# Kernel optimization log

Measured on AMD Instinct MI355X. Metric: run time of the kernel, lower is better.

The kernel has to match this reference:

```python
import jax, jax.numpy as jnp
import numpy as np

LN_EPS = 1e-5

def _layernorm(z, g, b):
    m = jnp.mean(z, axis=-1, keepdims=True)
    v = jnp.mean(jnp.square(z - m), axis=-1, keepdims=True)
    return (z - m) / jnp.sqrt(v + LN_EPS) * g + b

def setup_inputs() -> dict:
    key = jax.random.key(0)
    ks = jax.random.split(key, 8)
    B, N, C, H = 16, 1024, 384, 6
    Dff = 4 * C
    s = 0.02
    return {
        "x": jax.random.normal(ks[0], (B, N, C), dtype=jnp.float32),
        "ln1_g": jnp.ones((C,), jnp.float32),
        "ln1_b": jnp.zeros((C,), jnp.float32),
        "qkv_w": jax.random.normal(ks[1], (3 * C, C), jnp.float32) * s,
        "proj_w": jax.random.normal(ks[2], (C, C), jnp.float32) * s,
        "proj_b": jnp.zeros((C,), jnp.float32),
        "gate_h": jnp.ones((H,), jnp.float32),
        "ln2_g": jnp.ones((C,), jnp.float32),
        "ln2_b": jnp.zeros((C,), jnp.float32),
        "fc1_w": jax.random.normal(ks[3], (Dff, C), jnp.float32) * s,
        "fc1_b": jnp.zeros((Dff,), jnp.float32),
        "fc2_w": jax.random.normal(ks[4], (C, Dff), jnp.float32) * s,
        "fc2_b": jnp.zeros((C,), jnp.float32),
        "gate_mlp": jnp.ones((Dff,), jnp.float32),
    }

def reference(x, ln1_g, ln1_b, qkv_w, proj_w, proj_b, gate_h,
              ln2_g, ln2_b, fc1_w, fc1_b, fc2_w, fc2_b, gate_mlp):
    B, N, C = x.shape
    H = gate_h.shape[0]
    Dh = C // H
    scale = Dh ** -0.5

    # Attention branch
    h = _layernorm(x, ln1_g, ln1_b)
    qkv = (h @ qkv_w.T).reshape(B, N, 3, H, Dh).transpose(2, 0, 3, 1, 4)  # [3,B,H,N,Dh]
    q, k, v = qkv[0], qkv[1], qkv[2]
    attn = jax.nn.softmax(jnp.einsum('bhnd,bhmd->bhnm', q, k) * scale, axis=-1)  # [B,H,N,N]
    o = jnp.einsum('bhnm,bhmd->bhnd', attn, v)            # [B,H,N,Dh]
    o = o.transpose(0, 2, 1, 3) * gate_h[None, None, :, None]  # per-head gate
    o = o.reshape(B, N, C) @ proj_w.T + proj_b
    x = x + o

    # MLP branch (exact GELU, per-neuron gate)
    h2 = _layernorm(x, ln2_g, ln2_b)
    m = jax.nn.gelu(h2 @ fc1_w.T + fc1_b, approximate=False) * gate_mlp
    x = x + (m @ fc2_w.T + fc2_b)
    return x
```

## Files before the change

### kernel.cpp

```cpp
#include <hip/hip_runtime.h>
#include <hip/hip_bf16.h>
#include <cstdint>
#include <cstddef>

#define B_   16
#define N_   1024
#define C_   384
#define H_   6
#define DFF_ 1536
#define R_   16384

typedef __attribute__((ext_vector_type(8))) __bf16 bf16x8;
typedef __attribute__((ext_vector_type(4))) float  f32x4;
typedef __attribute__((ext_vector_type(8))) unsigned short u16x8;
typedef __attribute__((ext_vector_type(4))) unsigned short u16x4;

__device__ __forceinline__ float bf2f(unsigned short u){
    unsigned int x = ((unsigned int)u) << 16;
    return __builtin_bit_cast(float, x);
}
__device__ __forceinline__ unsigned short f2bf(float f){
    return __builtin_bit_cast(unsigned short, __float2bfloat16(f));
}
__device__ __forceinline__ unsigned int cvt_pk_bf16(float a, float b){
    unsigned int r;
    asm("v_cvt_pk_bf16_f32 %0, %1, %2" : "=v"(r) : "v"(a), "v"(b));
    return r;
}
__device__ __forceinline__ float fast_exp2(float x){
    float r;
    asm("v_exp_f32 %0, %1" : "=v"(r) : "v"(x));
    return r;
}
__device__ __forceinline__ void gload16(const void* g, void* l){
    __builtin_amdgcn_global_load_lds(
        (const __attribute__((address_space(1))) unsigned int*)g,
        (__attribute__((address_space(3))) unsigned int*)l, 16, 0, 0);
}
__device__ __forceinline__ float gelu_f(float u){
    float z  = fabsf(u) * 0.70710678118654752f;
    float t  = __builtin_amdgcn_rcpf(1.0f + 0.47047f*z);
    float e  = __expf(-z*z);
    float p  = t*(0.3480242f + t*(-0.0958798f + t*0.7478556f));
    float er = 1.0f - p*e;
    return 0.5f*u*(1.0f + copysignf(er, u));
}
__device__ __forceinline__ float ldv(const float* p, size_t i){ return p[i]; }
__device__ __forceinline__ float ldv(const __hip_bfloat16* p, size_t i){ return __bfloat162float(p[i]); }

__global__ __launch_bounds__(256) void ln1_cvt_kernel(
    const float* __restrict__ x, const float* __restrict__ g,
    const float* __restrict__ b, __hip_bfloat16* __restrict__ out,
    const float* __restrict__ i0, __hip_bfloat16* __restrict__ o0, int n0,
    const float* __restrict__ i1, __hip_bfloat16* __restrict__ o1, int n1,
    const float* __restrict__ i2, __hip_bfloat16* __restrict__ o2, int n2,
    const float* __restrict__ i3, __hip_bfloat16* __restrict__ o3, int n3)
{
    if (blockIdx.x < 4096){
        const int lane = threadIdx.x & 63;
        const int wave = threadIdx.x >> 6;
        const int row  = blockIdx.x*4 + wave;
        const float* xr = x + (size_t)row*C_;
        float v[6];
        float s = 0.f;
        #pragma unroll
        for (int i=0;i<6;i++){ v[i] = xr[lane + i*64]; s += v[i]; }
        #pragma unroll
        for (int m=1;m<64;m<<=1) s += __shfl_xor(s, m);
        const float mean = s * (1.0f/C_);
        float sq = 0.f;
        #pragma unroll
        for (int i=0;i<6;i++){ float d = v[i]-mean; sq += d*d; }
        #pragma unroll
        for (int m=1;m<64;m<<=1) sq += __shfl_xor(sq, m);
        const float rstd = rsqrtf(sq*(1.0f/C_) + 1e-5f);
        #pragma unroll
        for (int i=0;i<6;i++){
            int c = lane + i*64;
            out[(size_t)row*C_ + c] = __float2bfloat16((v[i]-mean)*rstd*g[c] + b[c]);
        }
    } else {
        const int total = n0+n1+n2+n3;
        for (int i = (blockIdx.x-4096)*blockDim.x + threadIdx.x; i < total; i += 1024*blockDim.x){
            int k = i;
            if (k < n0){ o0[k] = __float2bfloat16(i0[k]); continue; }
            k -= n0;
            if (k < n1){ o1[k] = __float2bfloat16(i1[k]); continue; }
            k -= n1;
            if (k < n2){ o2[k] = __float2bfloat16(i2[k]); continue; }
            k -= n2;
            o3[k] = __float2bfloat16(i3[k]);
        }
    }
}

template<typename T>
__global__ __launch_bounds__(256) void ln_kernel(
    const T* __restrict__ x, const float* __restrict__ g,
    const float* __restrict__ b, __hip_bfloat16* __restrict__ out)
{
    const int lane = threadIdx.x & 63;
    const int wave = threadIdx.x >> 6;
    const int row  = blockIdx.x*4 + wave;
    const T* xr = x + (size_t)row*C_;
    float v[6];
    float s = 0.f;
    #pragma unroll
    for (int i=0;i<6;i++){ v[i] = ldv(xr, lane + i*64); s += v[i]; }
    #pragma unroll
    for (int m=1;m<64;m<<=1) s += __shfl_xor(s, m);
    const float mean = s * (1.0f/C_);
    float sq = 0.f;
    #pragma unroll
    for (int i=0;i<6;i++){ float d = v[i]-mean; sq += d*d; }
    #pragma unroll
    for (int m=1;m<64;m<<=1) sq += __shfl_xor(sq, m);
    const float rstd = rsqrtf(sq*(1.0f/C_) + 1e-5f);
    #pragma unroll
    for (int i=0;i<6;i++){
        int c = lane + i*64;
        out[(size_t)row*C_ + c] = __float2bfloat16((v[i]-mean)*rstd*g[c] + b[c]);
    }
}

enum { EPI_QKV=0, EPI_PROJ=1, EPI_FC2=3 };


template<int EPI, int NCOLS>
__global__ __launch_bounds__(256, 2) void gemm_wres(
    const __hip_bfloat16* __restrict__ A,
    const __hip_bfloat16* __restrict__ Wt,
    const float* __restrict__ bias,
    const float* __restrict__ resid,
    const float* __restrict__ gate,
    __hip_bfloat16* __restrict__ outb)
{
    constexpr int NB = NCOLS/64;
    constexpr int G  = 24;
    __shared__ __align__(16) unsigned short As[4][128*32];
    __shared__ __align__(16) unsigned short Bs[64*384];
    const int t = threadIdx.x;
    const int l = t & 63;
    const int w = t >> 6;
    const int X  = blockIdx.x & 7;
    const int j8 = blockIdx.x >> 3;
    const int rb = X*8 + j8 / NB;
    const int cb = j8 % NB;

    #pragma unroll
    for (int j=0;j<12;j++){
        const int L     = (w*12 + j)*1024 + l*16;
        const int row   = L / 768;
        const int cbyte = L - row*768;
        const int scol  = (cbyte ^ ((row&7)<<4)) >> 1;
        gload16(Wt + (size_t)(cb*64 + row)*384 + scol, (char*)&Bs[0] + L);
    }
    const int sgcol = (((l&3) - ((l>>3)&3)) & 3) * 8;
    const size_t arow0 = (size_t)rb*256 + w*32 + (l>>2);
    auto STAGEA = [&](int g){
        const int rt = g/12, s = g - rt*12;
        #pragma unroll
        for (int c=0;c<2;c++)
            gload16(A + (arow0 + rt*128 + c*16)*384 + s*32 + sgcol,
                    (char*)&As[g&3][0] + w*2048 + c*1024 + l*16);
    };
    STAGEA(0); STAGEA(1); STAGEA(2);
    asm volatile("s_waitcnt vmcnt(6)" ::: "memory");
    __builtin_amdgcn_s_barrier();

    #pragma unroll
    for (int rt=0; rt<2; ++rt){
        f32x4 acc[2][4];
        #pragma unroll
        for (int i=0;i<2;i++)
            #pragma unroll
            for (int jj=0;jj<4;jj++) acc[i][jj] = (f32x4){0.f,0.f,0.f,0.f};

        #pragma unroll
        for (int s=0; s<12; ++s){
            const int g = rt*12 + s;
            if (g <= G-3)      asm volatile("s_waitcnt vmcnt(4)" ::: "memory");
            else if (g == G-2) asm volatile("s_waitcnt vmcnt(2)" ::: "memory");
            else               asm volatile("s_waitcnt vmcnt(0)" ::: "memory");
            const char* as = (const char*)&As[g&3][0] + w*2048;
            bf16x8 af[2], bw[4];
            #pragma unroll
            for (int i=0;i<2;i++){
                const int r  = i*16 + (l&15);
                const int sl = ((l>>4) + ((r>>1)&3)) & 3;
                af[i] = *(const bf16x8*)(as + r*64 + sl*16);
            }
            #pragma unroll
            for (int i=0;i<4;i++){
                const int r = i*16 + (l&15);
                bw[i] = *(const bf16x8*)((const char*)&Bs[0] + r*768
                             + ((s*64 + (l>>4)*16) ^ ((r&7)<<4)));
            }
            #pragma unroll
            for (int mi=0;mi<2;mi++)
                #pragma unroll
                for (int ni=0;ni<4;ni++)
                    acc[mi][ni] = __builtin_amdgcn_mfma_f32_16x16x32_bf16(af[mi], bw[ni], acc[mi][ni], 0,0,0);
            asm volatile("s_waitcnt lgkmcnt(0)" ::: "memory");
            if (g+3 < G) STAGEA(g+3);
        }
        const int rowBase = rb*256 + rt*128 + w*32;
        if constexpr (EPI==EPI_QKV){
            unsigned short* ob = (unsigned short*)outb;
            #pragma unroll
            for (int ni=0; ni<4; ni++){
                const int col = cb*64 + ni*16 + (l&15);
                const int p = col/384, rem = col - p*384;
                const int hh = rem>>6, d = rem&63;
                #pragma unroll
                for (int mi=0; mi<2; mi++){
                    const int row0 = rowBase + mi*16 + (l>>4)*4;
                    const int bb = row0>>10, n = row0&1023;
                    if (p==2){
                        u16x4 pk;
                        #pragma unroll
                        for (int jj=0;jj<4;jj++) pk[jj] = f2bf(acc[mi][ni][jj]);
                        *(u16x4*)(ob + (size_t)2*6291456 + ((size_t)(bb*H_+hh)*64 + d)*1024 + n) = pk;
                    } else {
                        #pragma unroll
                        for (int jj=0;jj<4;jj++)
                            ob[(((size_t)((p*16+bb)*6+hh))<<16) + ((size_t)(n+jj)<<6) + d] = f2bf(acc[mi][ni][jj]);
                    }
                }
            }
        } else {
            #pragma unroll
            for (int ni=0; ni<4; ni++){
                const int col = cb*64 + ni*16 + (l&15);
                #pragma unroll
                for (int mi=0; mi<2; mi++){
                    #pragma unroll
                    for (int jj=0;jj<4;jj++){
                        const int row = rowBase + mi*16 + (l>>4)*4 + jj;
                        const size_t idx = (size_t)row*NCOLS + col;
                        outb[idx] = __float2bfloat16(resid[idx] + acc[mi][ni][jj] + bias[col]);
                    }
                }
            }
        }
    }
}

template<int NCOLS>
__global__ __launch_bounds__(256, 2) void gemm_wres4(
    const __hip_bfloat16* __restrict__ A,
    const __hip_bfloat16* __restrict__ Wt,
    const float* __restrict__ bias,
    const float* __restrict__ gate,
    __hip_bfloat16* __restrict__ outb)
{
    constexpr int NB = NCOLS/64;
    __shared__ __align__(16) unsigned short As[4][128*32];
    __shared__ __align__(16) unsigned short Bs[64*384];
    const int t = threadIdx.x;
    const int l = t & 63;
    const int w = t >> 6;
    const int X  = blockIdx.x & 7;
    const int j8 = blockIdx.x >> 3;
    const int rb = X*16 + j8 / NB;
    const int cb = j8 % NB;

    #pragma unroll
    for (int j=0;j<12;j++){
        const int L     = (w*12 + j)*1024 + l*16;
        const int row   = L / 768;
        const int cbyte = L - row*768;
        const int scol  = (cbyte ^ ((row&7)<<4)) >> 1;
        gload16(Wt + (size_t)(cb*64 + row)*384 + scol, (char*)&Bs[0] + L);
    }
    const int sgcol = (((l&3) - ((l>>3)&3)) & 3) * 8;
    const size_t arow0 = (size_t)rb*128 + w*32 + (l>>2);
    auto STAGEA = [&](int g){
        #pragma unroll
        for (int c=0;c<2;c++)
            gload16(A + (arow0 + c*16)*384 + g*32 + sgcol,
                    (char*)&As[g&3][0] + w*2048 + c*1024 + l*16);
    };
    STAGEA(0); STAGEA(1); STAGEA(2);
    asm volatile("s_waitcnt vmcnt(6)" ::: "memory");
    __builtin_amdgcn_s_barrier();

    f32x4 acc[2][4];
    #pragma unroll
    for (int i=0;i<2;i++)
        #pragma unroll
        for (int jj=0;jj<4;jj++) acc[i][jj] = (f32x4){0.f,0.f,0.f,0.f};

    #pragma unroll
    for (int s=0; s<12; ++s){
        if (s < 10)      asm volatile("s_waitcnt vmcnt(4)" ::: "memory");
        else if (s == 10) asm volatile("s_waitcnt vmcnt(2)" ::: "memory");
        else              asm volatile("s_waitcnt vmcnt(0)" ::: "memory");
        const char* as = (const char*)&As[s&3][0] + w*2048;
        bf16x8 af[2], bw[4];
        #pragma unroll
        for (int i=0;i<2;i++){
            const int r  = i*16 + (l&15);
            const int sl = ((l>>4) + ((r>>1)&3)) & 3;
            af[i] = *(const bf16x8*)(as + r*64 + sl*16);
        }
        #pragma unroll
        for (int i=0;i<4;i++){
            const int r = i*16 + (l&15);
            bw[i] = *(const bf16x8*)((const char*)&Bs[0] + r*768
                         + ((s*64 + (l>>4)*16) ^ ((r&7)<<4)));
        }
        #pragma unroll
        for (int mi=0;mi<2;mi++)
            #pragma unroll
            for (int ni=0;ni<4;ni++)
                acc[mi][ni] = __builtin_amdgcn_mfma_f32_16x16x32_bf16(af[mi], bw[ni], acc[mi][ni], 0,0,0);
        asm volatile("s_waitcnt lgkmcnt(0)" ::: "memory");
        if (s+3 < 12) STAGEA(s+3);
    }

    const int rowBase = rb*128 + w*32;
    #pragma unroll
    for (int ni=0; ni<4; ni++){
        const int col = cb*64 + ni*16 + (l&15);
        #pragma unroll
        for (int mi=0; mi<2; mi++){
            #pragma unroll
            for (int jj=0;jj<4;jj++){
                const int row = rowBase + mi*16 + (l>>4)*4 + jj;
                const size_t idx = (size_t)row*NCOLS + col;
                outb[idx] = __float2bfloat16(gelu_f(acc[mi][ni][jj] + bias[col]) * gate[col]);
            }
        }
    }
}

__global__ __launch_bounds__(256, 2) void gemm_wres_fc2(
    const __hip_bfloat16* __restrict__ A,
    const __hip_bfloat16* __restrict__ Wt,
    const float* __restrict__ bias,
    const __hip_bfloat16* __restrict__ residb,
    float* __restrict__ outf)
{
    constexpr int NB = 6;
    __shared__ __align__(16) unsigned short As[4][128*32];
    __shared__ __align__(16) unsigned short Bs[64*384];
    const int t = threadIdx.x;
    const int l = t & 63;
    const int w = t >> 6;
    const int X  = blockIdx.x & 7;
    const int j8 = blockIdx.x >> 3;
    const int rb = X*16 + j8 / NB;
    const int cb = j8 % NB;

    auto STAGEB = [&](int q){
        #pragma unroll
        for (int j=0;j<12;j++){
            const int L     = (w*12 + j)*1024 + l*16;
            const int row   = L / 768;
            const int cbyte = L - row*768;
            const int scol  = (cbyte ^ ((row&7)<<4)) >> 1;
            gload16(Wt + (size_t)(cb*64 + row)*1536 + q*384 + scol, (char*)&Bs[0] + L);
        }
    };
    const int sgcol = (((l&3) - ((l>>3)&3)) & 3) * 8;
    const size_t arow0 = (size_t)rb*128 + w*32 + (l>>2);
    auto STAGEA = [&](int g){
        #pragma unroll
        for (int c=0;c<2;c++)
            gload16(A + (arow0 + c*16)*1536 + g*32 + sgcol,
                    (char*)&As[g&3][0] + w*2048 + c*1024 + l*16);
    };

    STAGEB(0);
    STAGEA(0); STAGEA(1); STAGEA(2);
    asm volatile("s_waitcnt vmcnt(0)" ::: "memory");
    __builtin_amdgcn_s_barrier();
    asm volatile("" ::: "memory");

    f32x4 acc[2][4];
    #pragma unroll
    for (int i=0;i<2;i++)
        #pragma unroll
        for (int jj=0;jj<4;jj++) acc[i][jj] = (f32x4){0.f,0.f,0.f,0.f};

    for (int q=0; q<4; ++q){
        if (q > 0){
            asm volatile("s_waitcnt vmcnt(0)" ::: "memory");
            __builtin_amdgcn_s_barrier();
            asm volatile("" ::: "memory");
        }
        #pragma unroll
        for (int s=0; s<12; ++s){
            const int g = q*12 + s;
            if (s >= 3){
                if (g < 46)      asm volatile("s_waitcnt vmcnt(4)" ::: "memory");
                else if (g == 46) asm volatile("s_waitcnt vmcnt(2)" ::: "memory");
                else              asm volatile("s_waitcnt vmcnt(0)" ::: "memory");
            }
            const char* as = (const char*)&As[g&3][0] + w*2048;
            bf16x8 af[2], bw[4];
            #pragma unroll
            for (int i=0;i<2;i++){
                const int r  = i*16 + (l&15);
                const int sl = ((l>>4) + ((r>>1)&3)) & 3;
                af[i] = *(const bf16x8*)(as + r*64 + sl*16);
            }
            #pragma unroll
            for (int i=0;i<4;i++){
                const int r = i*16 + (l&15);
                bw[i] = *(const bf16x8*)((const char*)&Bs[0] + r*768
                             + ((s*64 + (l>>4)*16) ^ ((r&7)<<4)));
            }
            #pragma unroll
            for (int mi=0;mi<2;mi++)
                #pragma unroll
                for (int ni=0;ni<4;ni++)
                    acc[mi][ni] = __builtin_amdgcn_mfma_f32_16x16x32_bf16(af[mi], bw[ni], acc[mi][ni], 0,0,0);
            asm volatile("s_waitcnt lgkmcnt(0)" ::: "memory");
            if (g+3 < 48) STAGEA(g+3);
        }
        if (q < 3){
            __builtin_amdgcn_s_barrier();
            asm volatile("" ::: "memory");
            STAGEB(q+1);
        }
    }

    const int rowBase = rb*128 + w*32;
    const unsigned short* xb = (const unsigned short*)residb;
    #pragma unroll
    for (int ni=0; ni<4; ni++){
        const int col = cb*64 + ni*16 + (l&15);
        #pragma unroll
        for (int mi=0; mi<2; mi++){
            #pragma unroll
            for (int jj=0;jj<4;jj++){
                const int row = rowBase + mi*16 + (l>>4)*4 + jj;
                const size_t idx = (size_t)row*384 + col;
                outf[idx] = bf2f(xb[idx]) + acc[mi][ni][jj] + bias[col];
            }
        }
    }
}

__global__ __launch_bounds__(256) void attn_mfma(
    const __hip_bfloat16* __restrict__ qg,
    const __hip_bfloat16* __restrict__ kg,
    const __hip_bfloat16* __restrict__ vtg,
    const float* __restrict__ gate_h,
    __hip_bfloat16* __restrict__ og)
{
    __shared__ __align__(16) unsigned short Ks [3][64*64];
    __shared__ __align__(16) unsigned short Vts[3][64*64];
    const int t = threadIdx.x;
    const int l = t & 63;
    const int w = t >> 6;
    const int X  = blockIdx.x & 7;
    const int j8 = blockIdx.x >> 3;
    const int bh = X*12 + (j8 >> 3);
    const int n0 = (j8 & 7) * 128;
    const int h  = bh % H_;
    const int b  = bh / H_;
    const unsigned short* qp  = (const unsigned short*)qg  + ((size_t)bh*N_ + n0 + w*32)*64;
    const unsigned short* kp  = (const unsigned short*)kg  + (size_t)bh*N_*64;
    const unsigned short* vtp = (const unsigned short*)vtg + (size_t)bh*64*N_;

    bf16x8 qf[2][2];
    #pragma unroll
    for (int mt=0;mt<2;mt++)
        #pragma unroll
        for (int dc=0;dc<2;dc++){
            u16x8 raw = *(const u16x8*)(qp + ((size_t)(mt*16 + (l&15)))*64 + dc*32 + (l>>4)*8);
            u16x8 sc;
            #pragma unroll
            for (int j=0;j<8;j++) sc[j] = f2bf(bf2f(raw[j]) * 0.1803368801111244f);
            qf[mt][dc] = __builtin_bit_cast(bf16x8, sc);
        }

    int qk_off[4][2], pv_off[2][4];
    #pragma unroll
    for (int t4=0;t4<4;t4++){
        const int i    = l & 15;
        const int row  = 8*(i>>2) + (i&3) + 4*(t4&1) + 32*(t4>>1);
        const int swzr = (row&3) | (((row>>3)&1)<<2);
        #pragma unroll
        for (int dc=0;dc<2;dc++)
            qk_off[t4][dc] = row*128 + ((dc*64 + (l>>4)*16) ^ (swzr<<4));
    }
    #pragma unroll
    for (int nt=0;nt<4;nt++){
        const int row  = nt*16 + (l&15);
        const int swzr = (row&3) | (((row>>3)&1)<<2);
        #pragma unroll
        for (int kc=0;kc<2;kc++)
            pv_off[kc][nt] = row*128 + ((kc*64 + (l>>4)*16) ^ (swzr<<4));
    }

    const int sr  = t >> 3;
    const int sce = (t & 7) * 8;

    auto STAGE = [&](int buf, int kt){
        #pragma unroll
        for (int c=0;c<2;c++){
            const int r    = sr + c*32;
            const int swzr = (r&3) | (((r>>3)&1)<<2);
            const int col  = sce ^ (swzr<<3);
            gload16(kp  + ((size_t)(kt*64 + r))*64 + col, (char*)&Ks [buf][0] + (c*256 + t)*16);
            gload16(vtp + (size_t)r*N_ + kt*64 + col,     (char*)&Vts[buf][0] + (c*256 + t)*16);
        }
    };

    f32x4 o_acc[2][4];
    #pragma unroll
    for (int i=0;i<2;i++)
        #pragma unroll
        for (int jj=0;jj<4;jj++) o_acc[i][jj] = (f32x4){0.f,0.f,0.f,0.f};
    float rs_part[2] = {0.f, 0.f};

    STAGE(0, 0);
    STAGE(1, 1);
    int cur = 0, stb = 2;
    for (int kt=0; kt<16; kt++){
        if (kt < 15) asm volatile("s_waitcnt vmcnt(4)" ::: "memory");
        else         asm volatile("s_waitcnt vmcnt(0)" ::: "memory");
        __builtin_amdgcn_s_barrier();
        asm volatile("" ::: "memory");
        if (kt < 14){
            STAGE(stb, kt+2);
            stb = (stb+1==3) ? 0 : stb+1;
        }
        const char* ks = (const char*)&Ks[cur][0];
        const char* vs = (const char*)&Vts[cur][0];

        f32x4 s_acc[4][2];
        #pragma unroll
        for (int i=0;i<4;i++)
            #pragma unroll
            for (int jj=0;jj<2;jj++) s_acc[i][jj] = (f32x4){0.f,0.f,0.f,0.f};
        #pragma unroll
        for (int t4=0;t4<4;t4++)
            #pragma unroll
            for (int dc=0;dc<2;dc++){
                bf16x8 kf = *(const bf16x8*)(ks + qk_off[t4][dc]);
                #pragma unroll
                for (int mt=0;mt<2;mt++)
                    s_acc[t4][mt] = __builtin_amdgcn_mfma_f32_16x16x32_bf16(kf, qf[mt][dc], s_acc[t4][mt], 0,0,0);
            }
        #pragma unroll
        for (int mt=0;mt<2;mt++){
            float acc_s = 0.f;
            #pragma unroll
            for (int t4=0;t4<4;t4++){
                #pragma unroll
                for (int jj=0;jj<4;jj++){
                    float e = fast_exp2(s_acc[t4][mt][jj]);
                    s_acc[t4][mt][jj] = e;
                    acc_s += e;
                }
            }
            rs_part[mt] += acc_s;
        }
        #pragma unroll
        for (int kc=0;kc<2;kc++){
            union { unsigned int u[4]; bf16x8 v; } pu[2];
            #pragma unroll
            for (int mt=0;mt<2;mt++){
                pu[mt].u[0] = cvt_pk_bf16(s_acc[2*kc  ][mt][0], s_acc[2*kc  ][mt][1]);
                pu[mt].u[1] = cvt_pk_bf16(s_acc[2*kc  ][mt][2], s_acc[2*kc  ][mt][3]);
                pu[mt].u[2] = cvt_pk_bf16(s_acc[2*kc+1][mt][0], s_acc[2*kc+1][mt][1]);
                pu[mt].u[3] = cvt_pk_bf16(s_acc[2*kc+1][mt][2], s_acc[2*kc+1][mt][3]);
            }
            #pragma unroll
            for (int nt=0;nt<4;nt++){
                bf16x8 vf = *(const bf16x8*)(vs + pv_off[kc][nt]);
                #pragma unroll
                for (int mt=0;mt<2;mt++)
                    o_acc[mt][nt] = __builtin_amdgcn_mfma_f32_16x16x32_bf16(pu[mt].v, vf, o_acc[mt][nt], 0,0,0);
            }
        }
        cur = (cur+1==3) ? 0 : cur+1;
    }
    float rowsum[2];
    #pragma unroll
    for (int mt=0;mt<2;mt++){
        float rs = rs_part[mt];
        rs += __shfl_xor(rs, 16);
        rs += __shfl_xor(rs, 32);
        rowsum[mt] = rs;
    }
    const float gh = gate_h[h];
    float inv[2][4];
    #pragma unroll
    for (int mt=0;mt<2;mt++)
        #pragma unroll
        for (int r=0;r<4;r++)
            inv[mt][r] = gh / __shfl(rowsum[mt], (l>>4)*4 + r, 16);
    unsigned short* op = (unsigned short*)og + ((size_t)b*N_ + n0 + w*32)*C_ + h*64;
    #pragma unroll
    for (int mt=0;mt<2;mt++){
        #pragma unroll
        for (int r=0;r<4;r++){
            const int n = mt*16 + (l>>4)*4 + r;
            #pragma unroll
            for (int nt=0;nt<4;nt++)
                op[(size_t)n*C_ + nt*16 + (l&15)] = f2bf(o_acc[mt][nt][r]*inv[mt][r]);
        }
    }
}

extern "C" void kernel_launch(void* const* d_in, const int* in_sizes, int n_in,
                              void* d_out, int out_size, void* d_ws, size_t ws_size,
                              hipStream_t stream)
{
    const float* x     = (const float*)d_in[0];
    const float* ln1g  = (const float*)d_in[1];
    const float* ln1b  = (const float*)d_in[2];
    const float* qkvw  = (const float*)d_in[3];
    const float* projw = (const float*)d_in[4];
    const float* projb = (const float*)d_in[5];
    const float* gateh = (const float*)d_in[6];
    const float* ln2g  = (const float*)d_in[7];
    const float* ln2b  = (const float*)d_in[8];
    const float* fc1w  = (const float*)d_in[9];
    const float* fc1b  = (const float*)d_in[10];
    const float* fc2w  = (const float*)d_in[11];
    const float* fc2b  = (const float*)d_in[12];
    const float* gatem = (const float*)d_in[13];
    float* out = (float*)d_out;

    char* ws = (char*)d_ws;
    __hip_bfloat16* h_buf = (__hip_bfloat16*)(ws + 0);
    __hip_bfloat16* qkv   = (__hip_bfloat16*)(ws + 12582912);
    __hip_bfloat16* q_buf = qkv;
    __hip_bfloat16* k_buf = qkv + 6291456;
    __hip_bfloat16* vt_buf= qkv + 2*6291456;
    __hip_bfloat16* o_buf = (__hip_bfloat16*)(ws + 50331648);
    __hip_bfloat16* m_buf = (__hip_bfloat16*)(ws + 12582912);
    __hip_bfloat16* x1b   = (__hip_bfloat16*)(ws + 62914560);
    __hip_bfloat16* wqkv  = (__hip_bfloat16*)(ws + 88080384);
    __hip_bfloat16* wproj = (__hip_bfloat16*)(ws + 88965120);
    __hip_bfloat16* wfc1  = (__hip_bfloat16*)(ws + 89260032);
    __hip_bfloat16* wfc2  = (__hip_bfloat16*)(ws + 90439680);

    ln1_cvt_kernel<<<5120, 256, 0, stream>>>(x, ln1g, ln1b, h_buf,
                                             qkvw, wqkv, 1152*384,
                                             projw, wproj, 384*384,
                                             fc1w, wfc1, 1536*384,
                                             fc2w, wfc2, 384*1536);

    gemm_wres<EPI_QKV,1152><<<1152, 256, 0, stream>>>(h_buf, wqkv, nullptr, nullptr, nullptr, qkv);
    attn_mfma<<<768, 256, 0, stream>>>(q_buf, k_buf, vt_buf, gateh, o_buf);
    gemm_wres<EPI_PROJ,384><<<384, 256, 0, stream>>>(o_buf, wproj, projb, x, nullptr, x1b);
    ln_kernel<__hip_bfloat16><<<4096, 256, 0, stream>>>(x1b, ln2g, ln2b, h_buf);
    gemm_wres4<1536><<<3072, 256, 0, stream>>>(h_buf, wfc1, fc1b, gatem, m_buf);
    gemm_wres_fc2<<<768, 256, 0, stream>>>(m_buf, wfc2, fc2b, x1b, out);
}
```

Baseline: 169.3 us.

## Unify FC1/FC2 GEMMs into a seven-buffer A pipeline with half-width B chunks

FC1 and FC2 now share one templated GEMM kernel. The weight tile is staged in 192-wide K chunks instead of 384, which frees LDS for seven A-tile buffers and lets A be prefetched six steps ahead instead of three. The fine-grained per-step vmcnt waits are replaced by one full wait plus barriers at each B-chunk boundary. FC1 therefore gains an extra mid-loop barrier and B reload. The coarser synchronisation may stall more often even though more loads are in flight.

New measurement: 174.6 us. 3.1% more time.

```diff
diff --git a/kernel.cpp b/kernel.cpp
--- a/kernel.cpp
+++ b/kernel.cpp
@@ -123,8 +123,7 @@
     }
 }
 
-enum { EPI_QKV=0, EPI_PROJ=1, EPI_FC2=3 };
-
+enum { EPI_QKV=0, EPI_PROJ=1, EPI_FC1=2, EPI_FC2=3 };
 
 template<int EPI, int NCOLS>
 __global__ __launch_bounds__(256, 2) void gemm_wres(
@@ -246,17 +245,21 @@
     }
 }
 
-template<int NCOLS>
-__global__ __launch_bounds__(256, 2) void gemm_wres4(
+template<int EPI, int KK, int NCOLS>
+__global__ __launch_bounds__(256, 2) void gemm_wres7(
     const __hip_bfloat16* __restrict__ A,
     const __hip_bfloat16* __restrict__ Wt,
     const float* __restrict__ bias,
+    const __hip_bfloat16* __restrict__ residb,
     const float* __restrict__ gate,
-    __hip_bfloat16* __restrict__ outb)
+    __hip_bfloat16* __restrict__ outb,
+    float* __restrict__ outf)
 {
-    constexpr int NB = NCOLS/64;
-    __shared__ __align__(16) unsigned short As[4][128*32];
-    __shared__ __align__(16) unsigned short Bs[64*384];
+    constexpr int NB     = NCOLS/64;
+    constexpr int NSTEPS = KK/32;
+    constexpr int QC     = KK/192;
+    __shared__ __align__(16) unsigned short As[7][128*32];
+    __shared__ __align__(16) unsigned short Bs[64*192];
     const int t = threadIdx.x;
     const int l = t & 63;
     const int w = t >> 6;
@@ -265,115 +268,27 @@
     const int rb = X*16 + j8 / NB;
     const int cb = j8 % NB;
 
-    #pragma unroll
-    for (int j=0;j<12;j++){
-        const int L     = (w*12 + j)*1024 + l*16;
-        const int row   = L / 768;
-        const int cbyte = L - row*768;
-        const int scol  = (cbyte ^ ((row&7)<<4)) >> 1;
-        gload16(Wt + (size_t)(cb*64 + row)*384 + scol, (char*)&Bs[0] + L);
-    }
-    const int sgcol = (((l&3) - ((l>>3)&3)) & 3) * 8;
-    const size_t arow0 = (size_t)rb*128 + w*32 + (l>>2);
-    auto STAGEA = [&](int g){
-        #pragma unroll
-        for (int c=0;c<2;c++)
-            gload16(A + (arow0 + c*16)*384 + g*32 + sgcol,
-                    (char*)&As[g&3][0] + w*2048 + c*1024 + l*16);
-    };
-    STAGEA(0); STAGEA(1); STAGEA(2);
-    asm volatile("s_waitcnt vmcnt(6)" ::: "memory");
-    __builtin_amdgcn_s_barrier();
-
-    f32x4 acc[2][4];
-    #pragma unroll
-    for (int i=0;i<2;i++)
-        #pragma unroll
-        for (int jj=0;jj<4;jj++) acc[i][jj] = (f32x4){0.f,0.f,0.f,0.f};
-
-    #pragma unroll
-    for (int s=0; s<12; ++s){
-        if (s < 10)      asm volatile("s_waitcnt vmcnt(4)" ::: "memory");
-        else if (s == 10) asm volatile("s_waitcnt vmcnt(2)" ::: "memory");
-        else              asm volatile("s_waitcnt vmcnt(0)" ::: "memory");
-        const char* as = (const char*)&As[s&3][0] + w*2048;
-        bf16x8 af[2], bw[4];
-        #pragma unroll
-        for (int i=0;i<2;i++){
-            const int r  = i*16 + (l&15);
-            const int sl = ((l>>4) + ((r>>1)&3)) & 3;
-            af[i] = *(const bf16x8*)(as + r*64 + sl*16);
-        }
-        #pragma unroll
-        for (int i=0;i<4;i++){
-            const int r = i*16 + (l&15);
-            bw[i] = *(const bf16x8*)((const char*)&Bs[0] + r*768
-                         + ((s*64 + (l>>4)*16) ^ ((r&7)<<4)));
-        }
-        #pragma unroll
-        for (int mi=0;mi<2;mi++)
-            #pragma unroll
-            for (int ni=0;ni<4;ni++)
-                acc[mi][ni] = __builtin_amdgcn_mfma_f32_16x16x32_bf16(af[mi], bw[ni], acc[mi][ni], 0,0,0);
-        asm volatile("s_waitcnt lgkmcnt(0)" ::: "memory");
-        if (s+3 < 12) STAGEA(s+3);
-    }
-
-    const int rowBase = rb*128 + w*32;
-    #pragma unroll
-    for (int ni=0; ni<4; ni++){
-        const int col = cb*64 + ni*16 + (l&15);
-        #pragma unroll
-        for (int mi=0; mi<2; mi++){
-            #pragma unroll
-            for (int jj=0;jj<4;jj++){
-                const int row = rowBase + mi*16 + (l>>4)*4 + jj;
-                const size_t idx = (size_t)row*NCOLS + col;
-                outb[idx] = __float2bfloat16(gelu_f(acc[mi][ni][jj] + bias[col]) * gate[col]);
-            }
-        }
-    }
-}
-
-__global__ __launch_bounds__(256, 2) void gemm_wres_fc2(
-    const __hip_bfloat16* __restrict__ A,
-    const __hip_bfloat16* __restrict__ Wt,
-    const float* __restrict__ bias,
-    const __hip_bfloat16* __restrict__ residb,
-    float* __restrict__ outf)
-{
-    constexpr int NB = 6;
-    __shared__ __align__(16) unsigned short As[4][128*32];
-    __shared__ __align__(16) unsigned short Bs[64*384];
-    const int t = threadIdx.x;
-    const int l = t & 63;
-    const int w = t >> 6;
-    const int X  = blockIdx.x & 7;
-    const int j8 = blockIdx.x >> 3;
-    const int rb = X*16 + j8 / NB;
-    const int cb = j8 % NB;
-
     auto STAGEB = [&](int q){
         #pragma unroll
-        for (int j=0;j<12;j++){
-            const int L     = (w*12 + j)*1024 + l*16;
-            const int row   = L / 768;
-            const int cbyte = L - row*768;
+        for (int j=0;j<6;j++){
+            const int L     = (w*6 + j)*1024 + l*16;
+            const int row   = L / 384;
+            const int cbyte = L - row*384;
             const int scol  = (cbyte ^ ((row&7)<<4)) >> 1;
-            gload16(Wt + (size_t)(cb*64 + row)*1536 + q*384 + scol, (char*)&Bs[0] + L);
+            gload16(Wt + (size_t)(cb*64 + row)*KK + q*192 + scol, (char*)&Bs[0] + L);
         }
     };
     const int sgcol = (((l&3) - ((l>>3)&3)) & 3) * 8;
     const size_t arow0 = (size_t)rb*128 + w*32 + (l>>2);
-    auto STAGEA = [&](int g){
+    auto STAGEA = [&](int g, int buf){
         #pragma unroll
         for (int c=0;c<2;c++)
-            gload16(A + (arow0 + c*16)*1536 + g*32 + sgcol,
-                    (char*)&As[g&3][0] + w*2048 + c*1024 + l*16);
+            gload16(A + (arow0 + c*16)*KK + g*32 + sgcol,
+                    (char*)&As[buf][0] + w*2048 + c*1024 + l*16);
     };
 
     STAGEB(0);
-    STAGEA(0); STAGEA(1); STAGEA(2);
+    STAGEA(0,0); STAGEA(1,1); STAGEA(2,2); STAGEA(3,3); STAGEA(4,4); STAGEA(5,5);
     asm volatile("s_waitcnt vmcnt(0)" ::: "memory");
     __builtin_amdgcn_s_barrier();
     asm volatile("" ::: "memory");
@@ -384,61 +299,75 @@
         #pragma unroll
         for (int jj=0;jj<4;jj++) acc[i][jj] = (f32x4){0.f,0.f,0.f,0.f};
 
-    for (int q=0; q<4; ++q){
-        if (q > 0){
+    int bidx = 0;
+    for (int q=0; q<QC; ++q){
+        #pragma unroll
+        for (int s=0; s<6; ++s){
+            const int g = q*6 + s;
+            const char* as = (const char*)&As[bidx][0] + w*2048;
+            bf16x8 af[2], bw[4];
+            #pragma unroll
+            for (int i=0;i<2;i++){
+                const int r  = i*16 + (l&15);
+                const int sl = ((l>>4) + ((r>>1)&3) ) & 3;
+                af[i] = *(const bf16x8*)(as + r*64 + sl*16);
+            }
+            #pragma unroll
+            for (int i=0;i<4;i++){
+                const int r = i*16 + (l&15);
+                bw[i] = *(const bf16x8*)((const char*)&Bs[0] + r*384
+                             + ((s*64 + (l>>4)*16) ^ ((r&7)<<4)));
+            }
+            #pragma unroll
+            for (int mi=0;mi<2;mi++)
+                #pragma unroll
+                for (int ni=0;ni<4;ni++)
+                    acc[mi][ni] = __builtin_amdgcn_mfma_f32_16x16x32_bf16(af[mi], bw[ni], acc[mi][ni], 0,0,0);
+            asm volatile("s_waitcnt lgkmcnt(0)" ::: "memory");
+            if (g+6 < NSTEPS){
+                const int sb = (bidx == 0) ? 6 : bidx-1;
+                STAGEA(g+6, sb);
+            }
+            bidx = (bidx+1 == 7) ? 0 : bidx+1;
+        }
+        if (q+1 < QC){
+            __builtin_amdgcn_s_barrier();
+            asm volatile("" ::: "memory");
+            STAGEB(q+1);
             asm volatile("s_waitcnt vmcnt(0)" ::: "memory");
             __builtin_amdgcn_s_barrier();
             asm volatile("" ::: "memory");
         }
-        #pragma unroll
-        for (int s=0; s<12; ++s){
-            const int g = q*12 + s;
-            if (s >= 3){
-                if (g < 46)      asm volatile("s_waitcnt vmcnt(4)" ::: "memory");
-                else if (g == 46) asm volatile("s_waitcnt vmcnt(2)" ::: "memory");
-                else              asm volatile("s_waitcnt vmcnt(0)" ::: "memory");
-            }
-            const char* as = (const char*)&As[g&3][0] + w*2048;
-            bf16x8 af[2], bw[4];
-            #pragma unroll
-            for (int i=0;i<2;i++){
-                const int r  = i*16 + (l&15);
-                const int sl = ((l>>4) + ((r>>1)&3)) & 3;
-                af[i] = *(const bf16x8*)(as + r*64 + sl*16);
-            }
-            #pragma unroll
-            for (int i=0;i<4;i++){
-                const int r = i*16 + (l&15);
-                bw[i] = *(const bf16x8*)((const char*)&Bs[0] + r*768
-                             + ((s*64 + (l>>4)*16) ^ ((r&7)<<4)));
-            }
-            #pragma unroll
-            for (int mi=0;mi<2;mi++)
-                #pragma unroll
-                for (int ni=0;ni<4;ni++)
-                    acc[mi][ni] = __builtin_amdgcn_mfma_f32_16x16x32_bf16(af[mi], bw[ni], acc[mi][ni], 0,0,0);
-            asm volatile("s_waitcnt lgkmcnt(0)" ::: "memory");
-            if (g+3 < 48) STAGEA(g+3);
-        }
-        if (q < 3){
-            __builtin_amdgcn_s_barrier();
-            asm volatile("" ::: "memory");
-            STAGEB(q+1);
-        }
     }
 
     const int rowBase = rb*128 + w*32;
-    const unsigned short* xb = (const unsigned short*)residb;
-    #pragma unroll
-    for (int ni=0; ni<4; ni++){
-        const int col = cb*64 + ni*16 + (l&15);
-        #pragma unroll
-        for (int mi=0; mi<2; mi++){
-            #pragma unroll
-            for (int jj=0;jj<4;jj++){
-                const int row = rowBase + mi*16 + (l>>4)*4 + jj;
-                const size_t idx = (size_t)row*384 + col;
-                outf[idx] = bf2f(xb[idx]) + acc[mi][ni][jj] + bias[col];
+    if constexpr (EPI==EPI_FC1){
+        #pragma unroll
+        for (int ni=0; ni<4; ni++){
+            const int col = cb*64 + ni*16 + (l&15);
+            #pragma unroll
+            for (int mi=0; mi<2; mi++){
+                #pragma unroll
+                for (int jj=0;jj<4;jj++){
+                    const int row = rowBase + mi*16 + (l>>4)*4 + jj;
+                    outb[(size_t)row*NCOLS + col] =
+                        __float2bfloat16(gelu_f(acc[mi][ni][jj] + bias[col]) * gate[col]);
+                }
+            }
+        }
+    } else {
+        const unsigned short* xb = (const unsigned short*)residb;
+        #pragma unroll
+        for (int ni=0; ni<4; ni++){
+            const int col = cb*64 + ni*16 + (l&15);
+            #pragma unroll
+            for (int mi=0; mi<2; mi++){
+                #pragma unroll
+                for (int jj=0;jj<4;jj++){
+                    const int row = rowBase + mi*16 + (l>>4)*4 + jj;
+                    const size_t idx = (size_t)row*384 + col;
+                    outf[idx] = bf2f(xb[idx]) + acc[mi][ni][jj] + bias[col];
+                }
             }
         }
     }
@@ -653,6 +582,6 @@
     attn_mfma<<<768, 256, 0, stream>>>(q_buf, k_buf, vt_buf, gateh, o_buf);
     gemm_wres<EPI_PROJ,384><<<384, 256, 0, stream>>>(o_buf, wproj, projb, x, nullptr, x1b);
     ln_kernel<__hip_bfloat16><<<4096, 256, 0, stream>>>(x1b, ln2g, ln2b, h_buf);
-    gemm_wres4<1536><<<3072, 256, 0, stream>>>(h_buf, wfc1, fc1b, gatem, m_buf);
-    gemm_wres_fc2<<<768, 256, 0, stream>>>(m_buf, wfc2, fc2b, x1b, out);
-}
+    gemm_wres7<EPI_FC1,384,1536><<<3072, 256, 0, stream>>>(h_buf, wfc1, fc1b, nullptr, gatem, m_buf, nullptr);
+    gemm_wres7<EPI_FC2,1536,384><<<768, 256, 0, stream>>>(m_buf, wfc2, fc2b, x1b, nullptr, nullptr, out);
+}
```
